# Kernel tuning notes

Measured on AMD Instinct MI355X. Metric: run time of the kernel, lower is better.

The kernel has to match this reference:

```python
import jax, jax.numpy as jnp
import numpy as np

EPS = 1e-5
GROUPS = 32


def _groupnorm(x, gamma, beta):
    B, C, H, W = x.shape
    xr = x.reshape(B, GROUPS, C // GROUPS, H, W)
    mu = xr.mean(axis=(2, 3, 4), keepdims=True)
    var = xr.var(axis=(2, 3, 4), keepdims=True)
    xn = ((xr - mu) * jax.lax.rsqrt(var + EPS)).reshape(B, C, H, W)
    return xn * gamma[None, :, None, None] + beta[None, :, None, None]


def _conv1x1(x, w, b):
    # x: [B,C,H,W], w: [Cout,Cin], b: [Cout]
    return jnp.einsum('bchw,oc->bohw', x, w) + b[None, :, None, None]


def setup_inputs() -> dict:
    key = jax.random.key(0)
    ks = jax.random.split(key, 11)
    B, C, H, W = 4, 64, 64, 64
    s = 0.05  # weight scale for well-conditioned softmax
    inp = {
        'x': jax.random.normal(ks[0], (B, C, H, W), jnp.float32),
        'gn_gamma': jnp.ones((C,), jnp.float32),
        'gn_beta': jnp.zeros((C,), jnp.float32),
        'wq': jax.random.normal(ks[1], (C, C), jnp.float32) * s,
        'bq': jnp.zeros((C,), jnp.float32),
        'wk': jax.random.normal(ks[2], (C, C), jnp.float32) * s,
        'bk': jnp.zeros((C,), jnp.float32),
        'wv': jax.random.normal(ks[3], (C, C), jnp.float32) * s,
        'bv': jnp.zeros((C,), jnp.float32),
        'wp': jax.random.normal(ks[4], (C, C), jnp.float32) * s,
        'bp': jnp.zeros((C,), jnp.float32),
    }
    return inp


def reference(x, gn_gamma, gn_beta, wq, bq, wk, bk, wv, bv, wp, bp):
    B, C, H, W = x.shape
    h = _groupnorm(x, gn_gamma, gn_beta)
    q = _conv1x1(h, wq, bq)
    k = _conv1x1(h, wk, bk)
    v = _conv1x1(h, wv, bv)
    # scores over all spatial positions: [B,H,W,H,W]
    scale = 1.0 / jnp.sqrt(jnp.asarray(C, x.dtype))
    w = jnp.einsum('bchw,bcHW->bhwHW', q, k) * scale
    w = jax.nn.softmax(w.reshape(B, H, W, H * W), axis=-1).reshape(B, H, W, H, W)
    h = jnp.einsum('bhwHW,bcHW->bchw', w, v)
    h = _conv1x1(h, wp, bp)
    return x + h
```

## Files before the change

### kernel.cpp

```cpp
#include <hip/hip_runtime.h>
#include <stdint.h>

#define Bn 4
#define Cn 64
#define Sn 4096
#define Gn 32

typedef float v4f __attribute__((ext_vector_type(4)));
typedef short v8s __attribute__((ext_vector_type(8)));
typedef short v4s __attribute__((ext_vector_type(4)));

#define MFMA16(a,b,c) __builtin_amdgcn_mfma_f32_16x16x32_bf16((a),(b),(c),0,0,0)

__device__ __forceinline__ float bf2f(uint16_t u){
  union { uint32_t i; float f; } x; x.i = ((uint32_t)u) << 16; return x.f;
}
__device__ __forceinline__ uint16_t f2bf(float f){
  union { float f; uint32_t i; } x; x.f = f;
  uint32_t r = x.i + 0x7fffu + ((x.i >> 16) & 1u);
  return (uint16_t)(r >> 16);
}
__device__ __forceinline__ v8s pack8(float4 a, float4 b){
  v8s r;
  r[0]=(short)f2bf(a.x); r[1]=(short)f2bf(a.y); r[2]=(short)f2bf(a.z); r[3]=(short)f2bf(a.w);
  r[4]=(short)f2bf(b.x); r[5]=(short)f2bf(b.y); r[6]=(short)f2bf(b.z); r[7]=(short)f2bf(b.w);
  return r;
}

__global__ __launch_bounds__(256) void gn_stats(const float* __restrict__ x,
                                                float* __restrict__ stats)
{
  const int tid = threadIdx.x;
  const float* base = x + (size_t)blockIdx.x * 8192;
  float sum = 0.f, sq = 0.f;
  #pragma unroll
  for (int i = 0; i < 8; ++i) {
    float4 v = *(const float4*)(base + ((i << 8) + tid)*4);
    sum += v.x + v.y + v.z + v.w;
    sq  += v.x*v.x + v.y*v.y + v.z*v.z + v.w*v.w;
  }
  #pragma unroll
  for (int off = 1; off < 64; off <<= 1) {
    sum += __shfl_xor(sum, off);
    sq  += __shfl_xor(sq, off);
  }
  __shared__ float red[8];
  const int w = tid >> 6;
  if ((tid & 63) == 0) { red[w] = sum; red[4+w] = sq; }
  __syncthreads();
  if (tid == 0) {
    float s = red[0]+red[1]+red[2]+red[3];
    float q = red[4]+red[5]+red[6]+red[7];
    float mean = s * (1.f/8192.f);
    float var  = q * (1.f/8192.f) - mean*mean;
    stats[blockIdx.x]       = mean;
    stats[128 + blockIdx.x] = rsqrtf(fmaxf(var, 0.f) + 1e-5f);
  }
}

__global__ __launch_bounds__(256) void gn_qkv(
    const float* __restrict__ xg, const float* __restrict__ gamma,
    const float* __restrict__ beta,
    const float* __restrict__ wq, const float* __restrict__ bq,
    const float* __restrict__ wk, const float* __restrict__ bk,
    const float* __restrict__ wv, const float* __restrict__ bv,
    const float* __restrict__ stats,
    uint16_t* __restrict__ Qg, uint16_t* __restrict__ Kg, uint16_t* __restrict__ Vg)
{
  __shared__ uint16_t Hs[16*72];
  const int tid  = threadIdx.x;
  const int w    = tid >> 6;
  const int lane = tid & 63;
  const int l15  = lane & 15;
  const int quad = lane >> 4;
  const int b      = blockIdx.x >> 8;
  const int s_base = (blockIdx.x & 255) << 4;

  {
    const int c = lane;
    const int g = c >> 1;
    const float mean = stats[b*Gn + g];
    const float rstd = stats[128 + b*Gn + g];
    const float ga = gamma[c], be = beta[c];
    float4 v = *(const float4*)(xg + ((size_t)b*Cn + c)*Sn + s_base + (w << 2));
    const int r0 = w << 2;
    Hs[(r0+0)*72 + c] = f2bf((v.x - mean)*rstd*ga + be);
    Hs[(r0+1)*72 + c] = f2bf((v.y - mean)*rstd*ga + be);
    Hs[(r0+2)*72 + c] = f2bf((v.z - mean)*rstd*ga + be);
    Hs[(r0+3)*72 + c] = f2bf((v.w - mean)*rstd*ga + be);
  }
  __syncthreads();

  v8s bh0 = *(const v8s*)(Hs + l15*72 + (quad << 3));
  v8s bh1 = *(const v8s*)(Hs + l15*72 + 32 + (quad << 3));

  #pragma unroll
  for (int t = 0; t < 3; ++t) {
    const int ot   = w*3 + t;
    const int wsel = ot >> 2;
    const int o16  = (ot & 3) << 4;
    const float* Wsel = (wsel == 0) ? wq : (wsel == 1) ? wk : wv;
    const float* Bsel = (wsel == 0) ? bq : (wsel == 1) ? bk : bv;
    const float* Wr = Wsel + (o16 + l15)*64 + (quad << 3);
    v8s a0 = pack8(*(const float4*)(Wr),      *(const float4*)(Wr + 4));
    v8s a1 = pack8(*(const float4*)(Wr + 32), *(const float4*)(Wr + 36));
    v4f d = (v4f){0.f,0.f,0.f,0.f};
    d = MFMA16(a0, bh0, d);
    d = MFMA16(a1, bh1, d);
    const int s = s_base + l15;
    if (wsel <= 1) {
      v4s qv;
      #pragma unroll
      for (int r = 0; r < 4; ++r)
        qv[r] = (short)f2bf(d[r] + Bsel[o16 + (quad << 2) + r]);
      uint16_t* dst = (wsel == 0 ? Qg : Kg) + ((size_t)b*Sn + s)*64 + o16 + (quad << 2);
      *(v4s*)dst = qv;
    } else {
      #pragma unroll
      for (int r = 0; r < 4; ++r) {
        const int o = o16 + (quad << 2) + r;
        Vg[((size_t)b*Cn + o)*Sn + s] = f2bf(d[r] + Bsel[o]);
      }
    }
  }
}

__global__ __launch_bounds__(256) void attn_split(
    const uint16_t* __restrict__ Qg, const uint16_t* __restrict__ Kg,
    const uint16_t* __restrict__ Vg,
    uint16_t* __restrict__ Opart, float* __restrict__ lpart)
{
  __shared__ uint16_t Ks[64*72];
  __shared__ uint16_t Vs[64*72];
  __shared__ uint16_t Ps[4][16*72];

  const int tid  = threadIdx.x;
  const int w    = tid >> 6;
  const int lane = tid & 63;
  const int l15  = lane & 15;
  const int quad = lane >> 4;
  const int bx    = blockIdx.x;
  const int split = bx & 3;
  const int qt    = (bx >> 2) & 63;
  const int b     = bx >> 8;
  const int i_base = qt << 6;
  const int j0     = split << 10;

  const uint16_t* Qb = Qg + ((size_t)b*Sn + i_base)*64;
  const uint16_t* Kb = Kg + (size_t)b*Sn*64;
  const uint16_t* Vb = Vg + (size_t)b*Cn*Sn;

  const int arow = (w << 4) + l15;
  v8s aq0 = *(const v8s*)(Qb + arow*64 + (quad << 3));
  v8s aq1 = *(const v8s*)(Qb + arow*64 + 32 + (quad << 3));

  const int e0 = tid << 3,        r0 = e0 >> 6, c0 = e0 & 63;
  const int e1 = (256 + tid) << 3, r1 = e1 >> 6, c1 = e1 & 63;

  *(v8s*)(Ks + r0*72 + c0) = *(const v8s*)(Kb + j0*64 + e0);
  *(v8s*)(Ks + r1*72 + c1) = *(const v8s*)(Kb + j0*64 + e1);
  *(v8s*)(Vs + r0*72 + c0) = *(const v8s*)(Vb + (size_t)r0*Sn + j0 + c0);
  *(v8s*)(Vs + r1*72 + c1) = *(const v8s*)(Vb + (size_t)r1*Sn + j0 + c1);

  float lsum[4];
  v4f o_acc[4];
  #pragma unroll
  for (int r = 0; r < 4; ++r) lsum[r] = 0.f;
  #pragma unroll
  for (int n = 0; n < 4; ++n) o_acc[n] = (v4f){0.f,0.f,0.f,0.f};

  __syncthreads();

  const float SC = 0.18033688011112042f;

  for (int kt = 0; kt < 16; ++kt) {
    v8s kp0, kp1, vp0, vp1;
    if (kt < 15) {
      const int jb = j0 + ((kt + 1) << 6);
      kp0 = *(const v8s*)(Kb + jb*64 + e0);
      kp1 = *(const v8s*)(Kb + jb*64 + e1);
      vp0 = *(const v8s*)(Vb + (size_t)r0*Sn + jb + c0);
      vp1 = *(const v8s*)(Vb + (size_t)r1*Sn + jb + c1);
    }

    v4f s[4];
    #pragma unroll
    for (int n = 0; n < 4; ++n) {
      const uint16_t* kr = Ks + ((n << 4) + l15)*72;
      v8s b0 = *(const v8s*)(kr + (quad << 3));
      v8s b1 = *(const v8s*)(kr + 32 + (quad << 3));
      v4f t = (v4f){0.f,0.f,0.f,0.f};
      t = MFMA16(aq0, b0, t);
      t = MFMA16(aq1, b1, t);
      s[n] = t;
    }

    uint16_t* Pw = Ps[w];
    #pragma unroll
    for (int n = 0; n < 4; ++n) {
      #pragma unroll
      for (int r = 0; r < 4; ++r) {
        const float pv = __builtin_amdgcn_exp2f(s[n][r]*SC);
        lsum[r] += pv;
        Pw[((quad << 2) + r)*72 + (n << 4) + l15] = f2bf(pv);
      }
    }

    __asm__ volatile("" ::: "memory");

    v8s ap0 = *(const v8s*)(Pw + l15*72 + (quad << 3));
    v8s ap1 = *(const v8s*)(Pw + l15*72 + 32 + (quad << 3));

    #pragma unroll
    for (int n = 0; n < 4; ++n) {
      const uint16_t* vrp = Vs + ((n << 4) + l15)*72;
      v8s b0 = *(const v8s*)(vrp + (quad << 3));
      v8s b1 = *(const v8s*)(vrp + 32 + (quad << 3));
      v4f o = o_acc[n];
      o = MFMA16(ap0, b0, o);
      o = MFMA16(ap1, b1, o);
      o_acc[n] = o;
    }

    __syncthreads();
    if (kt < 15) {
      *(v8s*)(Ks + r0*72 + c0) = kp0;
      *(v8s*)(Ks + r1*72 + c1) = kp1;
      *(v8s*)(Vs + r0*72 + c0) = vp0;
      *(v8s*)(Vs + r1*72 + c1) = vp1;
    }
    __syncthreads();
  }

  #pragma unroll
  for (int r = 0; r < 4; ++r) {
    lsum[r] += __shfl_xor(lsum[r], 1);
    lsum[r] += __shfl_xor(lsum[r], 2);
    lsum[r] += __shfl_xor(lsum[r], 4);
    lsum[r] += __shfl_xor(lsum[r], 8);
  }

  uint16_t* Ob = Opart + (size_t)bx*4096 + (w << 4)*64;
  float*    lp = lpart + bx*64 + (w << 4);
  #pragma unroll
  for (int n = 0; n < 4; ++n)
    #pragma unroll
    for (int r = 0; r < 4; ++r)
      Ob[((quad << 2) + r)*64 + (n << 4) + l15] = f2bf(o_acc[n][r]);
  if (l15 == 0) {
    #pragma unroll
    for (int r = 0; r < 4; ++r) lp[(quad << 2) + r] = lsum[r];
  }
}

__global__ __launch_bounds__(256) void proj_res(
    const uint16_t* __restrict__ Opart, const float* __restrict__ lpart,
    const float* __restrict__ wp, const float* __restrict__ bp,
    const float* __restrict__ xg, float* __restrict__ out)
{
  __shared__ uint16_t As[16*72];
  const int tid  = threadIdx.x;
  const int w    = tid >> 6;
  const int lane = tid & 63;
  const int l15  = lane & 15;
  const int quad = lane >> 4;
  const int b      = blockIdx.x >> 8;
  const int st     = blockIdx.x & 255;
  const int qt     = st >> 2;
  const int sub    = st & 3;
  const int s_base = st << 4;

  const uint16_t* po = Opart + (size_t)((b*64 + qt)*4)*4096 + (sub << 4)*64;
  const float*    pl = lpart + ((b*64 + qt)*4)*64 + (sub << 4);

  {
    const int e = tid << 2, row = tid >> 4, col = (tid & 15) << 2;
    const float linv = 1.f / (pl[row] + pl[64+row] + pl[128+row] + pl[192+row]);
    float acc[4] = {0.f,0.f,0.f,0.f};
    #pragma unroll
    for (int sp = 0; sp < 4; ++sp) {
      v4s o = *(const v4s*)(po + sp*4096 + e);
      #pragma unroll
      for (int j = 0; j < 4; ++j) acc[j] += bf2f((uint16_t)o[j]);
    }
    v4s a;
    #pragma unroll
    for (int j = 0; j < 4; ++j) a[j] = (short)f2bf(acc[j]*linv);
    *(v4s*)(As + row*72 + col) = a;
  }
  __syncthreads();

  v8s ba0 = *(const v8s*)(As + l15*72 + (quad << 3));
  v8s ba1 = *(const v8s*)(As + l15*72 + 32 + (quad << 3));

  const float* Wr = wp + ((w << 4) + l15)*64 + (quad << 3);
  v8s a0 = pack8(*(const float4*)(Wr),      *(const float4*)(Wr + 4));
  v8s a1 = pack8(*(const float4*)(Wr + 32), *(const float4*)(Wr + 36));
  v4f d = (v4f){0.f,0.f,0.f,0.f};
  d = MFMA16(a0, ba0, d);
  d = MFMA16(a1, ba1, d);
  const int s = s_base + l15;
  #pragma unroll
  for (int r = 0; r < 4; ++r) {
    const int o = (w << 4) + (quad << 2) + r;
    const size_t idx = ((size_t)b*Cn + o)*Sn + s;
    out[idx] = d[r] + bp[o] + xg[idx];
  }
}

extern "C" void kernel_launch(void* const* d_in, const int* in_sizes, int n_in,
                              void* d_out, int out_size, void* d_ws, size_t ws_size,
                              hipStream_t stream)
{
  const float* x     = (const float*)d_in[0];
  const float* gamma = (const float*)d_in[1];
  const float* beta  = (const float*)d_in[2];
  const float* wq    = (const float*)d_in[3];
  const float* bq    = (const float*)d_in[4];
  const float* wk    = (const float*)d_in[5];
  const float* bk    = (const float*)d_in[6];
  const float* wv    = (const float*)d_in[7];
  const float* bv    = (const float*)d_in[8];
  const float* wp    = (const float*)d_in[9];
  const float* bp    = (const float*)d_in[10];

  float*    stats = (float*)d_ws;
  uint16_t* Qg    = (uint16_t*)d_ws + 1024;
  uint16_t* Kg    = Qg + (size_t)Bn*Sn*Cn;
  uint16_t* Vg    = Kg + (size_t)Bn*Sn*Cn;
  uint16_t* Opart = Vg + (size_t)Bn*Sn*Cn;
  float*    lpart = (float*)(Opart + (size_t)1024*4096);
  float*    outp  = (float*)d_out;

  gn_stats  <<<128, 256, 0, stream>>>(x, stats);
  gn_qkv    <<<1024, 256, 0, stream>>>(x, gamma, beta, wq, bq, wk, bk, wv, bv,
                                       stats, Qg, Kg, Vg);
  attn_split<<<1024, 256, 0, stream>>>(Qg, Kg, Vg, Opart, lpart);
  proj_res  <<<1024, 256, 0, stream>>>(Opart, lpart, wp, bp, x, outp);
}
```

Before: 131.3 us.

## Compute transposed scores to keep P in registers and double-buffer K/V

The attention kernel now computes S^T (K as the A operand, Q as the B operand), so the exp'd probabilities come out already in the layout the PV MFMA expects. They are packed to bf16 with v_cvt_pk_bf16_f32 in registers, which removes the LDS round trip for P. Each wave now handles 32 query rows instead of 16, halving the grid to 512 blocks and raising reuse of each K/V tile. K/V LDS buffers are double-buffered, cutting one of the two barriers per iteration, and the softmax scale is folded into Q in the QKV kernel. The trade-offs are higher register pressure, fewer blocks for latency hiding, and a changed LDS read pattern for V.

```diff
diff --git a/kernel.cpp b/kernel.cpp
--- a/kernel.cpp
+++ b/kernel.cpp
@@ -19,6 +19,11 @@
   union { float f; uint32_t i; } x; x.f = f;
   uint32_t r = x.i + 0x7fffu + ((x.i >> 16) & 1u);
   return (uint16_t)(r >> 16);
+}
+__device__ __forceinline__ uint32_t cvtpk(float a, float b){
+  uint32_t r;
+  asm("v_cvt_pk_bf16_f32 %0, %1, %2" : "=v"(r) : "v"(a), "v"(b));
+  return r;
 }
 __device__ __forceinline__ v8s pack8(float4 a, float4 b){
   v8s r;
@@ -75,6 +80,7 @@
   const int quad = lane >> 4;
   const int b      = blockIdx.x >> 8;
   const int s_base = (blockIdx.x & 255) << 4;
+  const float QSC = 0.18033688011112042f;
 
   {
     const int c = lane;
@@ -111,8 +117,11 @@
     if (wsel <= 1) {
       v4s qv;
       #pragma unroll
-      for (int r = 0; r < 4; ++r)
-        qv[r] = (short)f2bf(d[r] + Bsel[o16 + (quad << 2) + r]);
+      for (int r = 0; r < 4; ++r) {
+        float val = d[r] + Bsel[o16 + (quad << 2) + r];
+        if (wsel == 0) val *= QSC;
+        qv[r] = (short)f2bf(val);
+      }
       uint16_t* dst = (wsel == 0 ? Qg : Kg) + ((size_t)b*Sn + s)*64 + o16 + (quad << 2);
       *(v4s*)dst = qv;
     } else {
@@ -130,9 +139,8 @@
     const uint16_t* __restrict__ Vg,
     uint16_t* __restrict__ Opart, float* __restrict__ lpart)
 {
-  __shared__ uint16_t Ks[64*72];
-  __shared__ uint16_t Vs[64*72];
-  __shared__ uint16_t Ps[4][16*72];
+  __shared__ uint16_t Ks[2][64*72];
+  __shared__ uint16_t Vs[2][64*72];
 
   const int tid  = threadIdx.x;
   const int w    = tid >> 6;
@@ -141,39 +149,42 @@
   const int quad = lane >> 4;
   const int bx    = blockIdx.x;
   const int split = bx & 3;
-  const int qt    = (bx >> 2) & 63;
-  const int b     = bx >> 8;
-  const int i_base = qt << 6;
+  const int qt    = (bx >> 2) & 31;
+  const int b     = bx >> 7;
+  const int i_base = qt << 7;
   const int j0     = split << 10;
 
   const uint16_t* Qb = Qg + ((size_t)b*Sn + i_base)*64;
   const uint16_t* Kb = Kg + (size_t)b*Sn*64;
   const uint16_t* Vb = Vg + (size_t)b*Cn*Sn;
 
-  const int arow = (w << 4) + l15;
-  v8s aq0 = *(const v8s*)(Qb + arow*64 + (quad << 3));
-  v8s aq1 = *(const v8s*)(Qb + arow*64 + 32 + (quad << 3));
-
-  const int e0 = tid << 3,        r0 = e0 >> 6, c0 = e0 & 63;
+  v8s qb[2][2];
+  #pragma unroll
+  for (int h = 0; h < 2; ++h) {
+    const int row = (w << 5) + (h << 4) + l15;
+    qb[h][0] = *(const v8s*)(Qb + row*64 + (quad << 3));
+    qb[h][1] = *(const v8s*)(Qb + row*64 + 32 + (quad << 3));
+  }
+
+  const int e0 = tid << 3,         r0 = e0 >> 6, c0 = e0 & 63;
   const int e1 = (256 + tid) << 3, r1 = e1 >> 6, c1 = e1 & 63;
 
-  *(v8s*)(Ks + r0*72 + c0) = *(const v8s*)(Kb + j0*64 + e0);
-  *(v8s*)(Ks + r1*72 + c1) = *(const v8s*)(Kb + j0*64 + e1);
-  *(v8s*)(Vs + r0*72 + c0) = *(const v8s*)(Vb + (size_t)r0*Sn + j0 + c0);
-  *(v8s*)(Vs + r1*72 + c1) = *(const v8s*)(Vb + (size_t)r1*Sn + j0 + c1);
-
-  float lsum[4];
-  v4f o_acc[4];
-  #pragma unroll
-  for (int r = 0; r < 4; ++r) lsum[r] = 0.f;
-  #pragma unroll
-  for (int n = 0; n < 4; ++n) o_acc[n] = (v4f){0.f,0.f,0.f,0.f};
+  *(v8s*)(Ks[0] + r0*72 + c0) = *(const v8s*)(Kb + j0*64 + e0);
+  *(v8s*)(Ks[0] + r1*72 + c1) = *(const v8s*)(Kb + j0*64 + e1);
+  *(v8s*)(Vs[0] + r0*72 + c0) = *(const v8s*)(Vb + (size_t)r0*Sn + j0 + c0);
+  *(v8s*)(Vs[0] + r1*72 + c1) = *(const v8s*)(Vb + (size_t)r1*Sn + j0 + c1);
+
+  float lsum[2] = {0.f, 0.f};
+  v4f o_acc[2][4];
+  #pragma unroll
+  for (int h = 0; h < 2; ++h)
+    #pragma unroll
+    for (int nc = 0; nc < 4; ++nc) o_acc[h][nc] = (v4f){0.f,0.f,0.f,0.f};
 
   __syncthreads();
 
-  const float SC = 0.18033688011112042f;
-
   for (int kt = 0; kt < 16; ++kt) {
+    const int cur = kt & 1;
     v8s kp0, kp1, vp0, vp1;
     if (kt < 15) {
       const int jb = j0 + ((kt + 1) << 6);
@@ -183,73 +194,83 @@
       vp1 = *(const v8s*)(Vb + (size_t)r1*Sn + jb + c1);
     }
 
-    v4f s[4];
+    v8s ka[4][2];
     #pragma unroll
     for (int n = 0; n < 4; ++n) {
-      const uint16_t* kr = Ks + ((n << 4) + l15)*72;
-      v8s b0 = *(const v8s*)(kr + (quad << 3));
-      v8s b1 = *(const v8s*)(kr + 32 + (quad << 3));
-      v4f t = (v4f){0.f,0.f,0.f,0.f};
-      t = MFMA16(aq0, b0, t);
-      t = MFMA16(aq1, b1, t);
-      s[n] = t;
-    }
-
-    uint16_t* Pw = Ps[w];
-    #pragma unroll
-    for (int n = 0; n < 4; ++n) {
-      #pragma unroll
-      for (int r = 0; r < 4; ++r) {
-        const float pv = __builtin_amdgcn_exp2f(s[n][r]*SC);
-        lsum[r] += pv;
-        Pw[((quad << 2) + r)*72 + (n << 4) + l15] = f2bf(pv);
-      }
-    }
-
-    __asm__ volatile("" ::: "memory");
-
-    v8s ap0 = *(const v8s*)(Pw + l15*72 + (quad << 3));
-    v8s ap1 = *(const v8s*)(Pw + l15*72 + 32 + (quad << 3));
-
-    #pragma unroll
-    for (int n = 0; n < 4; ++n) {
-      const uint16_t* vrp = Vs + ((n << 4) + l15)*72;
-      v8s b0 = *(const v8s*)(vrp + (quad << 3));
-      v8s b1 = *(const v8s*)(vrp + 32 + (quad << 3));
-      v4f o = o_acc[n];
-      o = MFMA16(ap0, b0, o);
-      o = MFMA16(ap1, b1, o);
-      o_acc[n] = o;
-    }
-
-    __syncthreads();
+      const uint16_t* kr = Ks[cur] + ((n << 4) + l15)*72;
+      ka[n][0] = *(const v8s*)(kr + (quad << 3));
+      ka[n][1] = *(const v8s*)(kr + 32 + (quad << 3));
+    }
+
+    v8s pa[2][2];
+    #pragma unroll
+    for (int h = 0; h < 2; ++h) {
+      v4f s[4];
+      #pragma unroll
+      for (int n = 0; n < 4; ++n) {
+        v4f t = (v4f){0.f,0.f,0.f,0.f};
+        t = MFMA16(ka[n][0], qb[h][0], t);
+        t = MFMA16(ka[n][1], qb[h][1], t);
+        s[n] = t;
+      }
+      union { v8s s8; uint32_t u[4]; } u0, u1;
+      #pragma unroll
+      for (int n = 0; n < 4; ++n) {
+        const float p0 = __builtin_amdgcn_exp2f(s[n][0]);
+        const float p1 = __builtin_amdgcn_exp2f(s[n][1]);
+        const float p2 = __builtin_amdgcn_exp2f(s[n][2]);
+        const float p3 = __builtin_amdgcn_exp2f(s[n][3]);
+        lsum[h] += (p0 + p1) + (p2 + p3);
+        const uint32_t w0 = cvtpk(p0, p1);
+        const uint32_t w1 = cvtpk(p2, p3);
+        if (n < 2) { u0.u[(n & 1)*2] = w0; u0.u[(n & 1)*2 + 1] = w1; }
+        else       { u1.u[(n & 1)*2] = w0; u1.u[(n & 1)*2 + 1] = w1; }
+      }
+      pa[h][0] = u0.s8;
+      pa[h][1] = u1.s8;
+    }
+
+    #pragma unroll
+    for (int nc = 0; nc < 4; ++nc) {
+      const uint16_t* vrow = Vs[cur] + ((nc << 4) + l15)*72;
+      #pragma unroll
+      for (int c = 0; c < 2; ++c) {
+        union { v8s s8; v4s h4[2]; } vb;
+        vb.h4[0] = *(const v4s*)(vrow + (c << 5) + (quad << 2));
+        vb.h4[1] = *(const v4s*)(vrow + (c << 5) + 16 + (quad << 2));
+        o_acc[0][nc] = MFMA16(pa[0][c], vb.s8, o_acc[0][nc]);
+        o_acc[1][nc] = MFMA16(pa[1][c], vb.s8, o_acc[1][nc]);
+      }
+    }
+
     if (kt < 15) {
-      *(v8s*)(Ks + r0*72 + c0) = kp0;
-      *(v8s*)(Ks + r1*72 + c1) = kp1;
-      *(v8s*)(Vs + r0*72 + c0) = vp0;
-      *(v8s*)(Vs + r1*72 + c1) = vp1;
-    }
-    __syncthreads();
-  }
-
-  #pragma unroll
-  for (int r = 0; r < 4; ++r) {
-    lsum[r] += __shfl_xor(lsum[r], 1);
-    lsum[r] += __shfl_xor(lsum[r], 2);
-    lsum[r] += __shfl_xor(lsum[r], 4);
-    lsum[r] += __shfl_xor(lsum[r], 8);
-  }
-
-  uint16_t* Ob = Opart + (size_t)bx*4096 + (w << 4)*64;
-  float*    lp = lpart + bx*64 + (w << 4);
-  #pragma unroll
-  for (int n = 0; n < 4; ++n)
-    #pragma unroll
-    for (int r = 0; r < 4; ++r)
-      Ob[((quad << 2) + r)*64 + (n << 4) + l15] = f2bf(o_acc[n][r]);
-  if (l15 == 0) {
-    #pragma unroll
-    for (int r = 0; r < 4; ++r) lp[(quad << 2) + r] = lsum[r];
+      const int nxt = cur ^ 1;
+      *(v8s*)(Ks[nxt] + r0*72 + c0) = kp0;
+      *(v8s*)(Ks[nxt] + r1*72 + c1) = kp1;
+      *(v8s*)(Vs[nxt] + r0*72 + c0) = vp0;
+      *(v8s*)(Vs[nxt] + r1*72 + c1) = vp1;
+      __syncthreads();
+    }
+  }
+
+  #pragma unroll
+  for (int h = 0; h < 2; ++h) {
+    lsum[h] += __shfl_xor(lsum[h], 16);
+    lsum[h] += __shfl_xor(lsum[h], 32);
+  }
+
+  uint16_t* Ob = Opart + (size_t)bx*8192 + (size_t)(w << 5)*64;
+  float*    lp = lpart + bx*128 + (w << 5);
+  #pragma unroll
+  for (int h = 0; h < 2; ++h)
+    #pragma unroll
+    for (int nc = 0; nc < 4; ++nc)
+      #pragma unroll
+      for (int r = 0; r < 4; ++r)
+        Ob[((h << 4) + (quad << 2) + r)*64 + (nc << 4) + l15] = f2bf(o_acc[h][nc][r]);
+  if (lane < 16) {
+    lp[l15]      = lsum[0];
+    lp[16 + l15] = lsum[1];
   }
 }
 
@@ -266,20 +287,20 @@
   const int quad = lane >> 4;
   const int b      = blockIdx.x >> 8;
   const int st     = blockIdx.x & 255;
-  const int qt     = st >> 2;
-  const int sub    = st & 3;
+  const int qt     = st >> 3;
+  const int sub    = st & 7;
   const int s_base = st << 4;
 
-  const uint16_t* po = Opart + (size_t)((b*64 + qt)*4)*4096 + (sub << 4)*64;
-  const float*    pl = lpart + ((b*64 + qt)*4)*64 + (sub << 4);
+  const uint16_t* po = Opart + (size_t)((b*32 + qt)*4)*8192 + (sub << 4)*64;
+  const float*    pl = lpart + ((b*32 + qt)*4)*128 + (sub << 4);
 
   {
     const int e = tid << 2, row = tid >> 4, col = (tid & 15) << 2;
-    const float linv = 1.f / (pl[row] + pl[64+row] + pl[128+row] + pl[192+row]);
+    const float linv = 1.f / (pl[row] + pl[128+row] + pl[256+row] + pl[384+row]);
     float acc[4] = {0.f,0.f,0.f,0.f};
     #pragma unroll
     for (int sp = 0; sp < 4; ++sp) {
-      v4s o = *(const v4s*)(po + sp*4096 + e);
+      v4s o = *(const v4s*)(po + (size_t)sp*8192 + e);
       #pragma unroll
       for (int j = 0; j < 4; ++j) acc[j] += bf2f((uint16_t)o[j]);
     }
@@ -329,12 +350,12 @@
   uint16_t* Kg    = Qg + (size_t)Bn*Sn*Cn;
   uint16_t* Vg    = Kg + (size_t)Bn*Sn*Cn;
   uint16_t* Opart = Vg + (size_t)Bn*Sn*Cn;
-  float*    lpart = (float*)(Opart + (size_t)1024*4096);
+  float*    lpart = (float*)(Opart + (size_t)512*8192);
   float*    outp  = (float*)d_out;
 
   gn_stats  <<<128, 256, 0, stream>>>(x, stats);
   gn_qkv    <<<1024, 256, 0, stream>>>(x, gamma, beta, wq, bq, wk, bk, wv, bv,
                                        stats, Qg, Kg, Vg);
-  attn_split<<<1024, 256, 0, stream>>>(Qg, Kg, Vg, Opart, lpart);
+  attn_split<<<512, 256, 0, stream>>>(Qg, Kg, Vg, Opart, lpart);
   proj_res  <<<1024, 256, 0, stream>>>(Opart, lpart, wp, bp, x, outp);
 }
```

Result: faster. 120.0 us (-8.6%).
